# Kernel tuning notes

Measured on AMD Instinct MI355X. Metric: run time of the kernel, lower is better.

The kernel has to match this reference:

```python
import jax, jax.numpy as jnp
import numpy as np

B, S, HIST = 2, 2048, 2048
H, HK, D = 16, 16, 128
DIM = H * D

def setup_inputs() -> dict:
    key = jax.random.key(0)
    ks = jax.random.split(key, 8)
    x = jax.random.normal(ks[0], (B, S, DIM), jnp.float32)
    prev_k = jax.random.normal(ks[1], (B, HIST, HK, D), jnp.float32)
    prev_v = jax.random.normal(ks[2], (B, HIST, HK, D), jnp.float32)
    # causal mask: history fully visible, causal within the current chunk
    q_pos = HIST + jnp.arange(S)
    k_pos = jnp.arange(HIST + S)
    mask = jnp.where(k_pos[None, :] <= q_pos[:, None], 0.0, -1e9).astype(jnp.float32)[None, None]
    sc = 0.02
    wq = jax.random.normal(ks[3], (DIM, DIM), jnp.float32) * sc
    wk = jax.random.normal(ks[4], (DIM, DIM), jnp.float32) * sc
    wv = jax.random.normal(ks[5], (DIM, DIM), jnp.float32) * sc
    wo = jax.random.normal(ks[6], (DIM, DIM), jnp.float32) * sc
    return {"x": x, "prev_k": prev_k, "prev_v": prev_v, "mask": mask,
            "wq": wq, "wk": wk, "wv": wv, "wo": wo}

def reference(x, prev_k, prev_v, mask, wq, wk, wv, wo):
    b, s, _ = x.shape
    # nn.Linear: y = x @ W^T, weights stored [out, in]
    xq = jnp.einsum('bsd,ed->bse', x, wq).reshape(b, s, H, D)
    xk = jnp.einsum('bsd,ed->bse', x, wk).reshape(b, s, HK, D)
    xv = jnp.einsum('bsd,ed->bse', x, wv).reshape(b, s, HK, D)
    k_all = jnp.concatenate([prev_k, xk], axis=1)  # [b, hist+s, hk, d]
    v_all = jnp.concatenate([prev_v, xv], axis=1)
    scores = jnp.einsum('bqhd,bkhd->bhqk', xq, k_all) / jnp.sqrt(jnp.float32(D))
    scores = scores + mask
    probs = jax.nn.softmax(scores.astype(jnp.float32), axis=-1).astype(xq.dtype)
    out = jnp.einsum('bhqk,bkhd->bqhd', probs, v_all).reshape(b, s, H * D)
    out = jnp.einsum('bse,de->bsd', out, wo)
    return out, k_all, v_all
```

## Files before the change

kernel.cpp:

```cpp
#include <hip/hip_runtime.h>
#include <math.h>

typedef __attribute__((ext_vector_type(8))) short bf16x8;
typedef __attribute__((ext_vector_type(4))) short bf16x4;
typedef __attribute__((ext_vector_type(4))) float f32x4;

#define SSCL (0.08838834764831845f * 1.4426950408889634f)

__device__ __forceinline__ short f2bf(float f) {
    union { float f; unsigned u; } x; x.f = f;
    unsigned r = x.u + 0x7fffu + ((x.u >> 16) & 1u);
    return (short)(r >> 16);
}
__device__ __forceinline__ unsigned pack2bf(float a, float b) {
    return ((unsigned)(unsigned short)f2bf(a)) | (((unsigned)(unsigned short)f2bf(b)) << 16);
}

typedef const __attribute__((address_space(1))) unsigned int* gas_ptr;
typedef __attribute__((address_space(3))) unsigned int* las_ptr;
__device__ __forceinline__ void async_copy16(const void* g, void* l) {
    __builtin_amdgcn_global_load_lds((gas_ptr)g, (las_ptr)l, 16, 0, 0);
}

__global__ __launch_bounds__(256)
void cvt_kernel(const float* __restrict__ src, short* __restrict__ dst, int n4) {
    int i = blockIdx.x * 256 + threadIdx.x;
    const int stride = gridDim.x * 256;
    for (; i < n4; i += stride) {
        float4 v = ((const float4*)src)[i];
        bf16x4 o;
        o[0] = f2bf(v.x); o[1] = f2bf(v.y); o[2] = f2bf(v.z); o[3] = f2bf(v.w);
        ((bf16x4*)dst)[i] = o;
    }
}

__global__ __launch_bounds__(256)
void cvt3_kernel(const float* __restrict__ s0, const float* __restrict__ s1,
                 const float* __restrict__ s2, short* __restrict__ d0,
                 short* __restrict__ d1, short* __restrict__ d2, int n4) {
    const float* src = (blockIdx.y == 0) ? s0 : ((blockIdx.y == 1) ? s1 : s2);
    short* dst = (blockIdx.y == 0) ? d0 : ((blockIdx.y == 1) ? d1 : d2);
    int i = blockIdx.x * 256 + threadIdx.x;
    const int stride = gridDim.x * 256;
    for (; i < n4; i += stride) {
        float4 v = ((const float4*)src)[i];
        bf16x4 o;
        o[0] = f2bf(v.x); o[1] = f2bf(v.y); o[2] = f2bf(v.z); o[3] = f2bf(v.w);
        ((bf16x4*)dst)[i] = o;
    }
}

template<int QKV>
__global__ __launch_bounds__(256)
void gemm_kernel(const short* __restrict__ A,
                 const short* __restrict__ B0, const short* __restrict__ B1,
                 const short* __restrict__ B2,
                 short* __restrict__ D16, float* __restrict__ Dk,
                 float* __restrict__ Dv, float* __restrict__ Df) {
    __shared__ short As[128 * 64];
    __shared__ short Bs[128 * 64];
    const int tid = threadIdx.x, w = tid >> 6, ln = tid & 63;
    const int col = ln & 15, quad = ln >> 4;
    const int sel = QKV ? (blockIdx.x >> 4) : 0;
    const int tn = (blockIdx.x & 15) * 128;
    const int tm = blockIdx.y * 128;
    const short* B = (sel == 0) ? B0 : ((sel == 1) ? B1 : B2);

    const int wm = (w >> 1) * 64, wn = (w & 1) * 64;
    const int srow = ln >> 3, scol = (ln & 7) * 8;

    f32x4 acc[4][4];
    for (int i = 0; i < 4; ++i)
        for (int j = 0; j < 4; ++j)
            for (int e = 0; e < 4; ++e) acc[i][j][e] = 0.f;

    for (int k0 = 0; k0 < 2048; k0 += 64) {
        #pragma unroll
        for (int i = 0; i < 4; ++i) {
            int chunk = i * 4 + w;
            int row = chunk * 8 + srow;
            async_copy16(&A[(tm + row) * 2048 + k0 + scol], &As[chunk * 512]);
            async_copy16(&B[(tn + row) * 2048 + k0 + scol], &Bs[chunk * 512]);
        }
        asm volatile("s_waitcnt vmcnt(0)" ::: "memory");
        __syncthreads();
        #pragma unroll
        for (int kk = 0; kk < 2; ++kk) {
            bf16x8 af[4], bfr[4];
            #pragma unroll
            for (int i = 0; i < 4; ++i)
                af[i] = *(const bf16x8*)&As[(wm + i * 16 + col) * 64 + kk * 32 + quad * 8];
            #pragma unroll
            for (int j = 0; j < 4; ++j)
                bfr[j] = *(const bf16x8*)&Bs[(wn + j * 16 + col) * 64 + kk * 32 + quad * 8];
            __builtin_amdgcn_s_setprio(1);
            #pragma unroll
            for (int i = 0; i < 4; ++i)
                #pragma unroll
                for (int j = 0; j < 4; ++j)
                    acc[i][j] = __builtin_amdgcn_mfma_f32_16x16x32_bf16(af[i], bfr[j], acc[i][j], 0, 0, 0);
            __builtin_amdgcn_s_setprio(0);
        }
        __syncthreads();
    }
    for (int i = 0; i < 4; ++i)
        for (int j = 0; j < 4; ++j)
            for (int r = 0; r < 4; ++r) {
                int m = tm + wm + i * 16 + quad * 4 + r;
                int n = tn + wn + j * 16 + col;
                float v = acc[i][j][r];
                if (QKV) {
                    if (sel == 0) {
                        D16[m * 2048 + n] = f2bf(v * SSCL);
                    } else {
                        int orow = m + ((m >> 11) + 1) * 2048;
                        float* D = (sel == 1) ? Dk : Dv;
                        D[orow * 2048 + n] = v;
                    }
                } else {
                    Df[m * 2048 + n] = v;
                }
            }
}

__global__ __launch_bounds__(256)
void prep_kv(const float* __restrict__ pk, const float* __restrict__ pv,
             float* __restrict__ Kall, float* __restrict__ Vall,
             short* __restrict__ Ktg, short* __restrict__ Vtg) {
    __shared__ short L[64 * 132];
    const int tid = threadIdx.x;
    const int k0 = blockIdx.x * 64;
    const int h = blockIdx.y, b = blockIdx.z;
    const bool hist = (k0 < 2048);
    const float* Ksrc = hist ? pk   + ((size_t)(b * 2048 + k0) * 16 + h) * 128
                             : Kall + ((size_t)(b * 4096 + k0) * 16 + h) * 128;
    const float* Vsrc = hist ? pv   + ((size_t)(b * 2048 + k0) * 16 + h) * 128
                             : Vall + ((size_t)(b * 4096 + k0) * 16 + h) * 128;
    float* Kdst = Kall + ((size_t)(b * 4096 + k0) * 16 + h) * 128;
    float* Vdst = Vall + ((size_t)(b * 4096 + k0) * 16 + h) * 128;
    short* Ko = Ktg + ((size_t)((b * 16 + h) * 4096) + k0) * 128;
    short* Vo = Vtg + ((size_t)(b * 16 + h) * 128) * 4096;
    #pragma unroll
    for (int i = 0; i < 8; ++i) {
        int idx = i * 256 + tid;
        int kr = idx >> 5, c4 = (idx & 31) * 4;
        float4 v = *(const float4*)&Ksrc[(size_t)kr * 2048 + c4];
        if (hist) *(float4*)&Kdst[(size_t)kr * 2048 + c4] = v;
        bf16x4 o4;
        o4[0] = f2bf(v.x); o4[1] = f2bf(v.y); o4[2] = f2bf(v.z); o4[3] = f2bf(v.w);
        *(bf16x4*)&Ko[(size_t)kr * 128 + (c4 ^ ((kr & 7) << 3))] = o4;
    }
    #pragma unroll
    for (int i = 0; i < 8; ++i) {
        int idx = i * 256 + tid;
        int r = idx >> 5, c4 = (idx & 31) * 4;
        float4 v = *(const float4*)&Vsrc[(size_t)r * 2048 + c4];
        if (hist) *(float4*)&Vdst[(size_t)r * 2048 + c4] = v;
        bf16x4 o4;
        o4[0] = f2bf(v.x); o4[1] = f2bf(v.y); o4[2] = f2bf(v.z); o4[3] = f2bf(v.w);
        *(bf16x4*)&L[r * 132 + c4] = o4;
    }
    __syncthreads();
    #pragma unroll
    for (int i = 0; i < 8; ++i) {
        int idx = i * 256 + tid;
        int d = idx >> 4, kc4 = (idx & 15) * 4;
        bf16x4 o4;
        o4[0] = L[(kc4 + 0) * 132 + d];
        o4[1] = L[(kc4 + 1) * 132 + d];
        o4[2] = L[(kc4 + 2) * 132 + d];
        o4[3] = L[(kc4 + 3) * 132 + d];
        *(bf16x4*)&Vo[(size_t)d * 4096 + k0 + (kc4 ^ ((d & 7) << 3))] = o4;
    }
}

__global__ __launch_bounds__(256)
void attn_mfma(const short* __restrict__ Q, const short* __restrict__ Ktg,
               const short* __restrict__ Vtg, short* __restrict__ Ot) {
    __shared__ short Ks[2][64 * 128];
    __shared__ short Vs[128 * 64];
    const int tid = threadIdx.x, w = tid >> 6, ln = tid & 63;
    const int col = ln & 15, quad = ln >> 4;
    const int bh = blockIdx.x;
    const int b = bh >> 4, h = bh & 15;
    const int s0 = blockIdx.y * 64;
    const int xk = (col & 7) << 3;

    bf16x8 qf[4];
    {
        const int qr = (b * 2048 + s0 + w * 16 + col) * 2048 + h * 128;
        #pragma unroll
        for (int ks = 0; ks < 4; ++ks)
            qf[ks] = *(const bf16x8*)&Q[qr + ks * 32 + quad * 8];
    }
    f32x4 o[8];
    #pragma unroll
    for (int i = 0; i < 8; ++i)
        for (int e = 0; e < 4; ++e) o[i][e] = 0.f;
    float m = -1e30f, l = 0.f;

    const short* Kb = Ktg + ((size_t)(b * 16 + h) * 4096) * 128;
    const short* Vb = Vtg + ((size_t)(b * 16 + h) * 128) * 4096;

    const int kr4 = ln >> 4;
    const int kc8 = (ln & 15) * 8;
    const int vd = (ln >> 3);
    const int vkofs = (ln & 7) * 8;

    const int ntiles = 33 + blockIdx.y;
    const int qp = 2048 + s0 + w * 16 + col;
    const int shsrcA = col + ((quad & 1) << 5);
    const bool qhi = (quad >> 1) != 0;

    #pragma unroll
    for (int i = 0; i < 4; ++i) {
        int ch = i * 4 + w;
        async_copy16(&Kb[(size_t)(ch * 4 + kr4) * 128 + kc8], &Ks[0][ch * 512]);
        async_copy16(&Vb[(size_t)(ch * 8 + vd) * 4096 + vkofs], &Vs[ch * 512]);
    }
    asm volatile("s_waitcnt vmcnt(0)" ::: "memory");
    __syncthreads();

    for (int t = 0; t < ntiles; ++t) {
        const int p = t & 1;
        const int k0 = t * 64;
        const bool pf = (t + 1 < ntiles);

        if (pf) {
            const int k0n = k0 + 64;
            #pragma unroll
            for (int i = 0; i < 4; ++i) {
                int ch = i * 4 + w;
                async_copy16(&Kb[(size_t)(k0n + ch * 4 + kr4) * 128 + kc8],
                             &Ks[p ^ 1][ch * 512]);
            }
        }

        f32x4 s4[4];
        #pragma unroll
        for (int j = 0; j < 4; ++j)
            for (int e = 0; e < 4; ++e) s4[j][e] = 0.f;
        #pragma unroll
        for (int ks = 0; ks < 4; ++ks) {
            const int dofs = (ks * 32 + quad * 8) ^ xk;
            bf16x8 kf[4];
            #pragma unroll
            for (int j = 0; j < 4; ++j)
                kf[j] = *(const bf16x8*)&Ks[p][(j * 16 + col) * 128 + dofs];
            __builtin_amdgcn_s_setprio(1);
            #pragma unroll
            for (int j = 0; j < 4; ++j)
                s4[j] = __builtin_amdgcn_mfma_f32_16x16x32_bf16(kf[j], qf[ks], s4[j], 0, 0, 0);
            __builtin_amdgcn_s_setprio(0);
        }

        const bool full = (k0 + 63 <= 2048 + s0 + w * 16);
        float pp[4][4];
        if (full) {
            #pragma unroll
            for (int j = 0; j < 4; ++j)
                #pragma unroll
                for (int r = 0; r < 4; ++r) pp[j][r] = s4[j][r];
        } else {
            #pragma unroll
            for (int j = 0; j < 4; ++j) {
                #pragma unroll
                for (int r = 0; r < 4; ++r) {
                    int kp = k0 + j * 16 + quad * 4 + r;
                    pp[j][r] = (kp <= qp) ? s4[j][r] : -1e30f;
                }
            }
        }
        float mx = pp[0][0];
        #pragma unroll
        for (int j = 0; j < 4; ++j)
            #pragma unroll
            for (int r = 0; r < 4; ++r) mx = fmaxf(mx, pp[j][r]);
        mx = fmaxf(mx, __shfl_xor(mx, 16));
        mx = fmaxf(mx, __shfl_xor(mx, 32));

        if (__all(mx <= m)) {
            float rs = 0.f;
            #pragma unroll
            for (int j = 0; j < 4; ++j)
                #pragma unroll
                for (int r = 0; r < 4; ++r) { pp[j][r] = exp2f(pp[j][r] - m); rs += pp[j][r]; }
            rs += __shfl_xor(rs, 16);
            rs += __shfl_xor(rs, 32);
            l += rs;
        } else {
            float mn = fmaxf(m, mx);
            float al = exp2f(m - mn);
            m = mn;
            float rs = 0.f;
            #pragma unroll
            for (int j = 0; j < 4; ++j)
                #pragma unroll
                for (int r = 0; r < 4; ++r) { pp[j][r] = exp2f(pp[j][r] - mn); rs += pp[j][r]; }
            rs += __shfl_xor(rs, 16);
            rs += __shfl_xor(rs, 32);
            l = l * al + rs;
            #pragma unroll
            for (int i = 0; i < 8; ++i)
                #pragma unroll
                for (int r = 0; r < 4; ++r) o[i][r] *= al;
        }

        unsigned u[4][2];
        #pragma unroll
        for (int j = 0; j < 4; ++j) {
            u[j][0] = pack2bf(pp[j][0], pp[j][1]);
            u[j][1] = pack2bf(pp[j][2], pp[j][3]);
        }
        unsigned pe[2][4];
        #pragma unroll
        for (int ks = 0; ks < 2; ++ks) {
            const int j0 = 2 * ks, j1 = 2 * ks + 1;
            unsigned A0 = (unsigned)__shfl((int)u[j0][0], shsrcA);
            unsigned A1 = (unsigned)__shfl((int)u[j0][1], shsrcA);
            unsigned A2 = (unsigned)__shfl((int)u[j1][0], shsrcA);
            unsigned A3 = (unsigned)__shfl((int)u[j1][1], shsrcA);
            unsigned B0 = (unsigned)__shfl((int)u[j0][0], shsrcA + 16);
            unsigned B1 = (unsigned)__shfl((int)u[j0][1], shsrcA + 16);
            unsigned B2 = (unsigned)__shfl((int)u[j1][0], shsrcA + 16);
            unsigned B3 = (unsigned)__shfl((int)u[j1][1], shsrcA + 16);
            pe[ks][0] = qhi ? A2 : A0;
            pe[ks][1] = qhi ? A3 : A1;
            pe[ks][2] = qhi ? B2 : B0;
            pe[ks][3] = qhi ? B3 : B1;
        }

        asm volatile("s_waitcnt vmcnt(0)" ::: "memory");
        __syncthreads();

        union { unsigned u4[4]; bf16x8 v8; } pb0, pb1;
        pb0.u4[0] = pe[0][0]; pb0.u4[1] = pe[0][1]; pb0.u4[2] = pe[0][2]; pb0.u4[3] = pe[0][3];
        pb1.u4[0] = pe[1][0]; pb1.u4[1] = pe[1][1]; pb1.u4[2] = pe[1][2]; pb1.u4[3] = pe[1][3];
        #pragma unroll
        for (int dt = 0; dt < 8; ++dt) {
            int row = dt * 16 + col;
            bf16x8 v0 = *(const bf16x8*)&Vs[row * 64 + ((quad * 8) ^ xk)];
            bf16x8 v1 = *(const bf16x8*)&Vs[row * 64 + ((32 + quad * 8) ^ xk)];
            __builtin_amdgcn_s_setprio(1);
            o[dt] = __builtin_amdgcn_mfma_f32_16x16x32_bf16(v0, pb0.v8, o[dt], 0, 0, 0);
            o[dt] = __builtin_amdgcn_mfma_f32_16x16x32_bf16(v1, pb1.v8, o[dt], 0, 0, 0);
            __builtin_amdgcn_s_setprio(0);
        }
        __syncthreads();

        if (pf) {
            const int k0n = k0 + 64;
            #pragma unroll
            for (int i = 0; i < 4; ++i) {
                int ch = i * 4 + w;
                async_copy16(&Vb[(size_t)(ch * 8 + vd) * 4096 + k0n + vkofs],
                             &Vs[ch * 512]);
            }
        }
    }
    const float inv = 1.f / l;
    const size_t ob = (size_t)(b * 2048 + s0 + w * 16 + col) * 2048 + h * 128 + quad * 4;
    #pragma unroll
    for (int dt = 0; dt < 8; ++dt) {
        bf16x4 q4;
        q4[0] = f2bf(o[dt][0] * inv);
        q4[1] = f2bf(o[dt][1] * inv);
        q4[2] = f2bf(o[dt][2] * inv);
        q4[3] = f2bf(o[dt][3] * inv);
        *(bf16x4*)&Ot[ob + dt * 16] = q4;
    }
}

extern "C" void kernel_launch(void* const* d_in, const int* in_sizes, int n_in,
                              void* d_out, int out_size, void* d_ws, size_t ws_size,
                              hipStream_t stream) {
    const float* x  = (const float*)d_in[0];
    const float* pk = (const float*)d_in[1];
    const float* pv = (const float*)d_in[2];
    const float* wq = (const float*)d_in[4];
    const float* wk = (const float*)d_in[5];
    const float* wv = (const float*)d_in[6];
    const float* wo = (const float*)d_in[7];

    float* out  = (float*)d_out;
    float* kall = out + 8388608;
    float* vall = out + 25165824;

    short* ws16 = (short*)d_ws;
    short* xb  = ws16;
    short* wqb = ws16 + 8388608;
    short* wkb = ws16 + 12582912;
    short* wvb = ws16 + 16777216;
    short* wob = ws16 + 20971520;
    short* vtg = ws16 + 8388608;
    short* qbf = ws16 + 25165824;
    short* ot  = xb;
    short* ktg = (short*)out;

    cvt_kernel<<<1024, 256, 0, stream>>>(x, xb, 2097152);
    cvt3_kernel<<<dim3(512, 3), 256, 0, stream>>>(wq, wk, wv, wqb, wkb, wvb, 1048576);

    gemm_kernel<1><<<dim3(48, 32), 256, 0, stream>>>(xb, wqb, wkb, wvb,
                                                     qbf, kall, vall, nullptr);
    prep_kv<<<dim3(64, 16, 2), 256, 0, stream>>>(pk, pv, kall, vall, ktg, vtg);
    attn_mfma<<<dim3(32, 32), 256, 0, stream>>>(qbf, ktg, vtg, ot);
    cvt_kernel<<<512, 256, 0, stream>>>(wo, wob, 1048576);
    gemm_kernel<0><<<dim3(16, 32), 256, 0, stream>>>(ot, wob, wob, wob,
                                                     nullptr, nullptr, nullptr, out);
}
```

Baseline: 770.5 us.

## Double-buffer V tiles in attention and merge input conversion launches

The attention kernel now keeps two V tile buffers in shared memory and prefetches the next V tile together with the next K tile. This removes the mid-iteration wait and barrier that previously exposed V load latency before the PV MFMAs. It costs an extra 16 KB of LDS per block, which may lower occupancy. Separately, the x conversion and the wq/wk/wv conversions are folded into a single launch to cut launch overhead.

```diff
diff --git a/kernel.cpp b/kernel.cpp
--- a/kernel.cpp
+++ b/kernel.cpp
@@ -35,11 +35,15 @@
 }
 
 __global__ __launch_bounds__(256)
-void cvt3_kernel(const float* __restrict__ s0, const float* __restrict__ s1,
-                 const float* __restrict__ s2, short* __restrict__ d0,
-                 short* __restrict__ d1, short* __restrict__ d2, int n4) {
-    const float* src = (blockIdx.y == 0) ? s0 : ((blockIdx.y == 1) ? s1 : s2);
-    short* dst = (blockIdx.y == 0) ? d0 : ((blockIdx.y == 1) ? d1 : d2);
+void cvt4_kernel(const float* __restrict__ s0, const float* __restrict__ s1,
+                 const float* __restrict__ s2, const float* __restrict__ s3,
+                 short* __restrict__ d0, short* __restrict__ d1,
+                 short* __restrict__ d2, short* __restrict__ d3,
+                 int n4x, int n4w) {
+    const int y = blockIdx.y;
+    const float* src = (y == 0) ? s0 : ((y == 1) ? s1 : ((y == 2) ? s2 : s3));
+    short* dst = (y == 0) ? d0 : ((y == 1) ? d1 : ((y == 2) ? d2 : d3));
+    const int n4 = (y == 0) ? n4x : n4w;
     int i = blockIdx.x * 256 + threadIdx.x;
     const int stride = gridDim.x * 256;
     for (; i < n4; i += stride) {
@@ -178,7 +182,7 @@
 void attn_mfma(const short* __restrict__ Q, const short* __restrict__ Ktg,
                const short* __restrict__ Vtg, short* __restrict__ Ot) {
     __shared__ short Ks[2][64 * 128];
-    __shared__ short Vs[128 * 64];
+    __shared__ short Vs[2][128 * 64];
     const int tid = threadIdx.x, w = tid >> 6, ln = tid & 63;
     const int col = ln & 15, quad = ln >> 4;
     const int bh = blockIdx.x;
@@ -216,7 +220,7 @@
     for (int i = 0; i < 4; ++i) {
         int ch = i * 4 + w;
         async_copy16(&Kb[(size_t)(ch * 4 + kr4) * 128 + kc8], &Ks[0][ch * 512]);
-        async_copy16(&Vb[(size_t)(ch * 8 + vd) * 4096 + vkofs], &Vs[ch * 512]);
+        async_copy16(&Vb[(size_t)(ch * 8 + vd) * 4096 + vkofs], &Vs[0][ch * 512]);
     }
     asm volatile("s_waitcnt vmcnt(0)" ::: "memory");
     __syncthreads();
@@ -233,6 +237,8 @@
                 int ch = i * 4 + w;
                 async_copy16(&Kb[(size_t)(k0n + ch * 4 + kr4) * 128 + kc8],
                              &Ks[p ^ 1][ch * 512]);
+                async_copy16(&Vb[(size_t)(ch * 8 + vd) * 4096 + k0n + vkofs],
+                             &Vs[p ^ 1][ch * 512]);
             }
         }
 
@@ -330,33 +336,22 @@
             pe[ks][3] = qhi ? B3 : B1;
         }
 
-        asm volatile("s_waitcnt vmcnt(0)" ::: "memory");
-        __syncthreads();
-
         union { unsigned u4[4]; bf16x8 v8; } pb0, pb1;
         pb0.u4[0] = pe[0][0]; pb0.u4[1] = pe[0][1]; pb0.u4[2] = pe[0][2]; pb0.u4[3] = pe[0][3];
         pb1.u4[0] = pe[1][0]; pb1.u4[1] = pe[1][1]; pb1.u4[2] = pe[1][2]; pb1.u4[3] = pe[1][3];
         #pragma unroll
         for (int dt = 0; dt < 8; ++dt) {
             int row = dt * 16 + col;
-            bf16x8 v0 = *(const bf16x8*)&Vs[row * 64 + ((quad * 8) ^ xk)];
-            bf16x8 v1 = *(const bf16x8*)&Vs[row * 64 + ((32 + quad * 8) ^ xk)];
+            bf16x8 v0 = *(const bf16x8*)&Vs[p][row * 64 + ((quad * 8) ^ xk)];
+            bf16x8 v1 = *(const bf16x8*)&Vs[p][row * 64 + ((32 + quad * 8) ^ xk)];
             __builtin_amdgcn_s_setprio(1);
             o[dt] = __builtin_amdgcn_mfma_f32_16x16x32_bf16(v0, pb0.v8, o[dt], 0, 0, 0);
             o[dt] = __builtin_amdgcn_mfma_f32_16x16x32_bf16(v1, pb1.v8, o[dt], 0, 0, 0);
             __builtin_amdgcn_s_setprio(0);
         }
+
+        asm volatile("s_waitcnt vmcnt(0)" ::: "memory");
         __syncthreads();
-
-        if (pf) {
-            const int k0n = k0 + 64;
-            #pragma unroll
-            for (int i = 0; i < 4; ++i) {
-                int ch = i * 4 + w;
-                async_copy16(&Vb[(size_t)(ch * 8 + vd) * 4096 + k0n + vkofs],
-                             &Vs[ch * 512]);
-            }
-        }
     }
     const float inv = 1.f / l;
     const size_t ob = (size_t)(b * 2048 + s0 + w * 16 + col) * 2048 + h * 128 + quad * 4;
@@ -397,8 +392,9 @@
     short* ot  = xb;
     short* ktg = (short*)out;
 
-    cvt_kernel<<<1024, 256, 0, stream>>>(x, xb, 2097152);
-    cvt3_kernel<<<dim3(512, 3), 256, 0, stream>>>(wq, wk, wv, wqb, wkb, wvb, 1048576);
+    cvt4_kernel<<<dim3(512, 4), 256, 0, stream>>>(x, wq, wk, wv,
+                                                  xb, wqb, wkb, wvb,
+                                                  2097152, 1048576);
 
     gemm_kernel<1><<<dim3(48, 32), 256, 0, stream>>>(xb, wqb, wkb, wvb,
                                                      qbf, kall, vall, nullptr);
```

New measurement: 769.1 us. About the same (-0.2%).
